# Kernel tuning notes

Hardware: AMD Instinct MI355X
Metric: run time of the kernel (lower is better)

## Reference

```python
import jax, jax.numpy as jnp
import numpy as np

HEADS = 16
DIM_HEAD = 64
QUERY_DIM = 1024
INNER = HEADS * DIM_HEAD
SCALE = DIM_HEAD ** -0.5


def setup_inputs() -> dict:
    key = jax.random.key(0)
    ks = jax.random.split(key, 6)
    B, N, M = 2, 2048, 2048
    x = jax.random.normal(ks[0], (B, N, QUERY_DIM), dtype=jnp.float32)
    context = jax.random.normal(ks[1], (B, M, QUERY_DIM), dtype=jnp.float32)
    s = QUERY_DIM ** -0.5
    # weights stored [in, out] so y = x @ W matches torch Linear(x) with W = weight.T
    Wq = jax.random.normal(ks[2], (QUERY_DIM, INNER), dtype=jnp.float32) * s
    Wk = jax.random.normal(ks[3], (QUERY_DIM, INNER), dtype=jnp.float32) * s
    Wv = jax.random.normal(ks[4], (QUERY_DIM, INNER), dtype=jnp.float32) * s
    Wo = jax.random.normal(ks[5], (INNER, QUERY_DIM), dtype=jnp.float32) * (INNER ** -0.5)
    return {"x": x, "context": context, "Wq": Wq, "Wk": Wk, "Wv": Wv, "Wo": Wo}


def reference(x, context, Wq, Wk, Wv, Wo):
    B, N, _ = x.shape
    M = context.shape[1]
    # projections -> [b, n, h, d]
    q = (x @ Wq).reshape(B, N, HEADS, DIM_HEAD)
    k = (context @ Wk).reshape(B, M, HEADS, DIM_HEAD)
    v = (context @ Wv).reshape(B, M, HEADS, DIM_HEAD)
    sim = jnp.einsum('bihd,bjhd->bhij', q, k) * SCALE  # [b, h, n, m]
    attn = jax.nn.softmax(sim, axis=-1)
    out = jnp.einsum('bhij,bjhd->bihd', attn, v)  # [b, n, h, d]
    out = out.reshape(B, N, INNER)
    return out @ Wo
```

## Files before the change

kernel.cpp:

```cpp
#include <hip/hip_runtime.h>
#include <hip/hip_bf16.h>


typedef __attribute__((ext_vector_type(8))) __bf16    bf16x8;
typedef __attribute__((ext_vector_type(4))) __bf16    bf16x4;
typedef __attribute__((ext_vector_type(4))) float     f32x4;

#define B_    2
#define H_    16
#define N_    2048
#define M_    2048
#define D_    64
#define QD_   1024

#define QSCALE 0.18033688011112042f

__device__ __forceinline__ void gld16(const __bf16* g, __bf16* l) {
    __builtin_amdgcn_global_load_lds(
        (const __attribute__((address_space(1))) unsigned int*)(g),
        (__attribute__((address_space(3))) unsigned int*)(l), 16, 0, 0);
}

__global__ __launch_bounds__(256) void cvt2_f32_bf16(const float* __restrict__ x,
                                                     const float* __restrict__ ctx,
                                                     __bf16* __restrict__ xb,
                                                     __bf16* __restrict__ cb) {
    const float* src = blockIdx.y ? ctx : x;
    __bf16*      dst = blockIdx.y ? cb  : xb;
    int i = (blockIdx.x * 256 + threadIdx.x) * 4;
    float4 v = *reinterpret_cast<const float4*>(src + i);
    bf16x4 o;
    o.x = (__bf16)v.x; o.y = (__bf16)v.y; o.z = (__bf16)v.z; o.w = (__bf16)v.w;
    *reinterpret_cast<bf16x4*>(dst + i) = o;
}

__global__ __launch_bounds__(256) void transpose4_cvt(const float* __restrict__ w0,
                                                      const float* __restrict__ w1,
                                                      const float* __restrict__ w2,
                                                      const float* __restrict__ w3,
                                                      __bf16* __restrict__ t0,
                                                      __bf16* __restrict__ t1,
                                                      __bf16* __restrict__ t2,
                                                      __bf16* __restrict__ t3) {
    __shared__ float tile[64][65];
    const int z = blockIdx.z;
    const float* in = (z == 0) ? w0 : (z == 1) ? w1 : (z == 2) ? w2 : w3;
    __bf16*     out = (z == 0) ? t0 : (z == 1) ? t1 : (z == 2) ? t2 : t3;
    const int i0 = blockIdx.x * 64;
    const int o0 = blockIdx.y * 64;
    const int t  = threadIdx.x;
    const int r  = t >> 4;
    const int c4 = (t & 15) * 4;
#pragma unroll
    for (int p = 0; p < 4; ++p) {
        int row = p * 16 + r;
        float4 v = *reinterpret_cast<const float4*>(in + (size_t)(i0 + row) * QD_ + o0 + c4);
        tile[row][c4 + 0] = v.x; tile[row][c4 + 1] = v.y;
        tile[row][c4 + 2] = v.z; tile[row][c4 + 3] = v.w;
    }
    __syncthreads();
#pragma unroll
    for (int p = 0; p < 4; ++p) {
        int orow = p * 16 + r;
        bf16x4 o;
        o.x = (__bf16)tile[c4 + 0][orow];
        o.y = (__bf16)tile[c4 + 1][orow];
        o.z = (__bf16)tile[c4 + 2][orow];
        o.w = (__bf16)tile[c4 + 3][orow];
        *reinterpret_cast<bf16x4*>(out + (size_t)(o0 + orow) * QD_ + i0 + c4) = o;
    }
}

#define GEMM_BODY(A_, Bt_)                                                                     \
    __shared__ __align__(16) __bf16 Alds[2][128 * 32];                                         \
    __shared__ __align__(16) __bf16 Blds[2][128 * 32];                                         \
    const int tid  = threadIdx.x;                                                              \
    const int wid  = tid >> 6;                                                                 \
    const int lane = tid & 63;                                                                 \
    const int l15  = lane & 15;                                                                \
    const int lg   = lane >> 4;                                                                \
    const int wr   = wid >> 1;                                                                 \
    const int wc   = wid & 1;                                                                  \
    const int rowBase = blockIdx.x * 128;                                                      \
    const int colBase = blockIdx.y * 128;                                                      \
    const int srow = wid * 32 + (lane >> 2);                                                   \
    const int skc  = (lane & 3) * 8;                                                           \
    const __bf16* Ag  = A_  + (size_t)(rowBase + srow) * QD_ + skc;                            \
    const __bf16* Ag2 = Ag  + (size_t)16 * QD_;                                                \
    const __bf16* Bg  = Bt_ + (size_t)(colBase + srow) * QD_ + skc;                            \
    const __bf16* Bg2 = Bg  + (size_t)16 * QD_;                                                \
    const int sOff  = (wid * 32) * 32;                                                         \
    const int sOff2 = sOff + 16 * 32;                                                          \
    f32x4 acc[4][4] = {};                                                                      \
    gld16(Ag,  &Alds[0][sOff]);                                                                \
    gld16(Ag2, &Alds[0][sOff2]);                                                               \
    gld16(Bg,  &Blds[0][sOff]);                                                                \
    gld16(Bg2, &Blds[0][sOff2]);                                                               \
    __syncthreads();                                                                           \
    for (int t = 0; t < 32; t += 2) {                                                          \
        if (t + 1 < 32) {                                                                      \
            int kn = (t + 1) * 32;                                                             \
            gld16(Ag + kn,  &Alds[1][sOff]);                                                   \
            gld16(Ag2 + kn, &Alds[1][sOff2]);                                                  \
            gld16(Bg + kn,  &Blds[1][sOff]);                                                   \
            gld16(Bg2 + kn, &Blds[1][sOff2]);                                                  \
        }                                                                                      \
        GCOMPUTE(0)                                                                            \
        __syncthreads();                                                                       \
        if (t + 2 < 32) {                                                                      \
            int kn = (t + 2) * 32;                                                             \
            gld16(Ag + kn,  &Alds[0][sOff]);                                                   \
            gld16(Ag2 + kn, &Alds[0][sOff2]);                                                  \
            gld16(Bg + kn,  &Blds[0][sOff]);                                                   \
            gld16(Bg2 + kn, &Blds[0][sOff2]);                                                  \
        }                                                                                      \
        GCOMPUTE(1)                                                                            \
        __syncthreads();                                                                      \
    }

#define GCOMPUTE(BUF)                                                                          \
    {                                                                                          \
        bf16x8 a[4], b[4];                                                                     \
        _Pragma("unroll")                                                                      \
        for (int m = 0; m < 4; ++m)                                                            \
            a[m] = *reinterpret_cast<const bf16x8*>(&Alds[BUF][(wr * 64 + m * 16 + l15) * 32 + lg * 8]); \
        _Pragma("unroll")                                                                      \
        for (int n = 0; n < 4; ++n)                                                            \
            b[n] = *reinterpret_cast<const bf16x8*>(&Blds[BUF][(wc * 64 + n * 16 + l15) * 32 + lg * 8]); \
        _Pragma("unroll")                                                                      \
        for (int m = 0; m < 4; ++m)                                                            \
            _Pragma("unroll")                                                                  \
            for (int n = 0; n < 4; ++n)                                                        \
                acc[m][n] = __builtin_amdgcn_mfma_f32_16x16x32_bf16(a[m], b[n], acc[m][n], 0, 0, 0); \
    }

__global__ __launch_bounds__(256) void gemm_qkv(const __bf16* __restrict__ xb,
                                                const __bf16* __restrict__ cb,
                                                const __bf16* __restrict__ Wtq,
                                                const __bf16* __restrict__ Wtk,
                                                const __bf16* __restrict__ Wtv,
                                                __bf16* __restrict__ Qb,
                                                __bf16* __restrict__ Kb,
                                                __bf16* __restrict__ Vt) {
    const int z = blockIdx.z;
    const __bf16* Asel = (z == 0) ? xb : cb;
    const __bf16* Bsel = (z == 0) ? Wtq : (z == 1) ? Wtk : Wtv;
    GEMM_BODY(Asel, Bsel)
#pragma unroll
    for (int m = 0; m < 4; ++m)
#pragma unroll
        for (int n = 0; n < 4; ++n)
#pragma unroll
            for (int r = 0; r < 4; ++r) {
                int rr = rowBase + wr * 64 + m * 16 + lg * 4 + r;
                int cc = colBase + wc * 64 + n * 16 + l15;
                float v = acc[m][n][r];
                int b_ = rr >> 11, nn = rr & 2047, hh = cc >> 6, dd = cc & 63;
                if (z == 0) {
                    Qb[((size_t)(b_ * H_ + hh) * N_ + nn) * D_ + dd] = (__bf16)(v * QSCALE);
                } else if (z == 1) {
                    Kb[((size_t)(b_ * H_ + hh) * N_ + nn) * D_ + dd] = (__bf16)v;
                } else {
                    Vt[((size_t)(b_ * H_ + hh) * D_ + dd) * M_ + nn] = (__bf16)v;
                }
            }
}

__global__ __launch_bounds__(256) void gemm_out(const __bf16* __restrict__ AO,
                                                const __bf16* __restrict__ Wto,
                                                float* __restrict__ out) {
    GEMM_BODY(AO, Wto)
#pragma unroll
    for (int m = 0; m < 4; ++m)
#pragma unroll
        for (int n = 0; n < 4; ++n)
#pragma unroll
            for (int r = 0; r < 4; ++r) {
                int rr = rowBase + wr * 64 + m * 16 + lg * 4 + r;
                int cc = colBase + wc * 64 + n * 16 + l15;
                out[(size_t)rr * QD_ + cc] = acc[m][n][r];
            }
}

__global__ __launch_bounds__(512, 4) void attn_kernel(const __bf16* __restrict__ Q,
                                                      const __bf16* __restrict__ K,
                                                      const __bf16* __restrict__ Vt,
                                                      __bf16* __restrict__ AO) {
    __shared__ __align__(16) __bf16 Klds[2][4096];
    __shared__ __align__(16) __bf16 Vlds[2][4096];

    const int logical = (blockIdx.x & 7) * 64 + (blockIdx.x >> 3);
    const int qt   = logical & 15;
    const int bh   = logical >> 4;
    const int b    = bh >> 4;
    const int h    = bh & 15;
    const int wid  = threadIdx.x >> 6;
    const int lane = threadIdx.x & 63;
    const int l15  = lane & 15;
    const int lg   = lane >> 4;
    const int qbase = qt * 128 + wid * 16;

    const __bf16* Qp = Q  + ((size_t)bh * N_ + qbase) * D_;
    const __bf16* Kp = K  + (size_t)bh * M_ * D_;
    const __bf16* Vp = Vt + (size_t)bh * D_ * M_;

    const int rg   = lane >> 3;
    const int ch   = lane & 7;
    const int skw  = (rg & 3) | ((wid & 1) << 2);
    const int kc   = (ch ^ skw) << 3;
    const int vc   = (ch ^ rg) << 3;
    const int srow = wid * 8 + rg;
    const int ldst = wid * 512;

#define STAGE(BUF, KV0)                                                        \
    gld16(Kp + (size_t)((KV0) + srow) * D_ + kc, &Klds[BUF][ldst]);            \
    gld16(Vp + (size_t)srow * M_ + (KV0) + vc,  &Vlds[BUF][ldst]);

    const int rm0 = ((l15 >> 2) * 8) + (l15 & 3);
    const int sq  = (l15 & 7) << 3;
    const int ak00 = rm0 * 64 + (( 0 + lg * 8) ^ sq);
    const int ak01 = rm0 * 64 + ((32 + lg * 8) ^ sq);
    const int ak10 = ak00 + 256;
    const int ak11 = ak01 + 256;
    const int av0 = l15 * 64 + (( 0 + lg * 8) ^ sq);
    const int av1 = l15 * 64 + ((32 + lg * 8) ^ sq);

    bf16x8 qf0 = *reinterpret_cast<const bf16x8*>(Qp + (size_t)l15 * D_ +      lg * 8);
    bf16x8 qf1 = *reinterpret_cast<const bf16x8*>(Qp + (size_t)l15 * D_ + 32 + lg * 8);

    bf16x8 onesf;
#pragma unroll
    for (int j = 0; j < 8; ++j) onesf[j] = (__bf16)1.0f;

    f32x4 o0 = {}, o1 = {}, o2 = {}, o3 = {}, ors = {};

#define COMPUTE(KB, VB, KOFF, AV)                                                               \
    {                                                                                           \
        bf16x8 k00 = *reinterpret_cast<const bf16x8*>((KB) + ak00 + (KOFF));                    \
        bf16x8 k01 = *reinterpret_cast<const bf16x8*>((KB) + ak01 + (KOFF));                    \
        bf16x8 k10 = *reinterpret_cast<const bf16x8*>((KB) + ak10 + (KOFF));                    \
        bf16x8 k11 = *reinterpret_cast<const bf16x8*>((KB) + ak11 + (KOFF));                    \
        bf16x8 v0  = *reinterpret_cast<const bf16x8*>((VB) + (AV));                             \
        bf16x8 v1  = *reinterpret_cast<const bf16x8*>((VB) + (AV) + 1024);                      \
        bf16x8 v2  = *reinterpret_cast<const bf16x8*>((VB) + (AV) + 2048);                      \
        bf16x8 v3  = *reinterpret_cast<const bf16x8*>((VB) + (AV) + 3072);                      \
        f32x4 s0 = {}, s1 = {};                                                                 \
        s0 = __builtin_amdgcn_mfma_f32_16x16x32_bf16(k00, qf0, s0, 0, 0, 0);                    \
        s0 = __builtin_amdgcn_mfma_f32_16x16x32_bf16(k01, qf1, s0, 0, 0, 0);                    \
        s1 = __builtin_amdgcn_mfma_f32_16x16x32_bf16(k10, qf0, s1, 0, 0, 0);                    \
        s1 = __builtin_amdgcn_mfma_f32_16x16x32_bf16(k11, qf1, s1, 0, 0, 0);                    \
        bf16x8 pf;                                                                              \
        pf[0] = (__bf16)__builtin_amdgcn_exp2f(s0[0]);                                          \
        pf[1] = (__bf16)__builtin_amdgcn_exp2f(s0[1]);                                          \
        pf[2] = (__bf16)__builtin_amdgcn_exp2f(s0[2]);                                          \
        pf[3] = (__bf16)__builtin_amdgcn_exp2f(s0[3]);                                          \
        pf[4] = (__bf16)__builtin_amdgcn_exp2f(s1[0]);                                          \
        pf[5] = (__bf16)__builtin_amdgcn_exp2f(s1[1]);                                          \
        pf[6] = (__bf16)__builtin_amdgcn_exp2f(s1[2]);                                          \
        pf[7] = (__bf16)__builtin_amdgcn_exp2f(s1[3]);                                          \
        ors = __builtin_amdgcn_mfma_f32_16x16x32_bf16(pf, onesf, ors, 0, 0, 0);                 \
        o0 = __builtin_amdgcn_mfma_f32_16x16x32_bf16(pf, v0, o0, 0, 0, 0);                      \
        o1 = __builtin_amdgcn_mfma_f32_16x16x32_bf16(pf, v1, o1, 0, 0, 0);                      \
        o2 = __builtin_amdgcn_mfma_f32_16x16x32_bf16(pf, v2, o2, 0, 0, 0);                      \
        o3 = __builtin_amdgcn_mfma_f32_16x16x32_bf16(pf, v3, o3, 0, 0, 0);                      \
    }

    STAGE(0, 0)
    __syncthreads();

    for (int t = 0; t < 32; t += 2) {
        if (t + 1 < 32) { STAGE(1, (t + 1) * 64) }
        COMPUTE(Klds[0], Vlds[0], 0,    av0)
        COMPUTE(Klds[0], Vlds[0], 2048, av1)
        __syncthreads();
        if (t + 2 < 32) { STAGE(0, (t + 2) * 64) }
        COMPUTE(Klds[1], Vlds[1], 0,    av0)
        COMPUTE(Klds[1], Vlds[1], 2048, av1)
        __syncthreads();
    }
#undef STAGE
#undef COMPUTE

#pragma unroll
    for (int r = 0; r < 4; ++r) {
        float inv = 1.0f / ors[r];
        size_t row = ((size_t)b * N_ + qbase + lg * 4 + r) * QD_ + h * D_ + l15;
        AO[row +  0] = (__bf16)(o0[r] * inv);
        AO[row + 16] = (__bf16)(o1[r] * inv);
        AO[row + 32] = (__bf16)(o2[r] * inv);
        AO[row + 48] = (__bf16)(o3[r] * inv);
    }
}

extern "C" void kernel_launch(void* const* d_in, const int* in_sizes, int n_in,
                              void* d_out, int out_size, void* d_ws, size_t ws_size,
                              hipStream_t stream) {
    const float* x   = (const float*)d_in[0];
    const float* ctx = (const float*)d_in[1];
    const float* Wq  = (const float*)d_in[2];
    const float* Wk  = (const float*)d_in[3];
    const float* Wv  = (const float*)d_in[4];
    const float* Wo  = (const float*)d_in[5];

    char* ws = (char*)d_ws;
    __bf16* xb  = (__bf16*)(ws);
    __bf16* cb  = (__bf16*)(ws + (8u  << 20));
    __bf16* Wtq = (__bf16*)(ws + (16u << 20));
    __bf16* Wtk = (__bf16*)(ws + (18u << 20));
    __bf16* Wtv = (__bf16*)(ws + (20u << 20));
    __bf16* Wto = (__bf16*)(ws + (22u << 20));
    __bf16* Qb  = (__bf16*)(ws + (24u << 20));
    __bf16* Kb  = (__bf16*)(ws + (32u << 20));
    __bf16* Vt  = (__bf16*)(ws + (40u << 20));
    __bf16* AO  = (__bf16*)(ws + (48u << 20));

    cvt2_f32_bf16<<<dim3(4096, 2), 256, 0, stream>>>(x, ctx, xb, cb);
    transpose4_cvt<<<dim3(16, 16, 4), 256, 0, stream>>>(Wq, Wk, Wv, Wo, Wtq, Wtk, Wtv, Wto);
    gemm_qkv<<<dim3(32, 8, 3), 256, 0, stream>>>(xb, cb, Wtq, Wtk, Wtv, Qb, Kb, Vt);
    attn_kernel<<<512, 512, 0, stream>>>(Qb, Kb, Vt, AO);
    gemm_out<<<dim3(32, 8), 256, 0, stream>>>(AO, Wto, (float*)d_out);
}
```

Before: 123.1 us.

## Load GEMM B fragments directly from global into registers and swizzle A LDS

The GEMM no longer stages the B (weight) tile through LDS. Each wave loads its B MFMA fragments straight from global memory into registers, double-buffered across k-steps. The A tile's LDS layout gains an XOR swizzle on the 16-byte column chunk to reduce bank conflicts on fragment reads. This halves LDS traffic and footprint, at the cost of redundant global B loads across the two row-waves and extra VGPR pressure.

After: 161.1 us. 1.31x slower.

```diff
diff --git a/kernel.cpp b/kernel.cpp
--- a/kernel.cpp
+++ b/kernel.cpp
@@ -73,7 +73,6 @@
 
 #define GEMM_BODY(A_, Bt_)                                                                     \
     __shared__ __align__(16) __bf16 Alds[2][128 * 32];                                         \
-    __shared__ __align__(16) __bf16 Blds[2][128 * 32];                                         \
     const int tid  = threadIdx.x;                                                              \
     const int wid  = tid >> 6;                                                                 \
     const int lane = tid & 63;                                                                 \
@@ -84,54 +83,65 @@
     const int rowBase = blockIdx.x * 128;                                                      \
     const int colBase = blockIdx.y * 128;                                                      \
     const int srow = wid * 32 + (lane >> 2);                                                   \
-    const int skc  = (lane & 3) * 8;                                                           \
-    const __bf16* Ag  = A_  + (size_t)(rowBase + srow) * QD_ + skc;                            \
-    const __bf16* Ag2 = Ag  + (size_t)16 * QD_;                                                \
-    const __bf16* Bg  = Bt_ + (size_t)(colBase + srow) * QD_ + skc;                            \
-    const __bf16* Bg2 = Bg  + (size_t)16 * QD_;                                                \
+    const int sg   = (((lane & 3) ^ ((srow >> 1) & 3))) * 8;     \
+    const __bf16* Ag  = A_  + (size_t)(rowBase + srow) * QD_ + sg;                             \
+    const __bf16* Ag2 = Ag  + (size_t)16 * QD_;           \
+    const __bf16* Bg  = Bt_ + (size_t)(colBase + wc * 64 + l15) * QD_ + lg * 8;                \
     const int sOff  = (wid * 32) * 32;                                                         \
     const int sOff2 = sOff + 16 * 32;                                                          \
+    int aoff[4];                                                                               \
+    _Pragma("unroll")                                                                          \
+    for (int m = 0; m < 4; ++m) {                                                              \
+        int row = wr * 64 + m * 16 + l15;                                                      \
+        aoff[m] = row * 32 + ((lg ^ ((row >> 1) & 3)) * 8);                                    \
+    }                                                                                          \
     f32x4 acc[4][4] = {};                                                                      \
+    bf16x8 bA0, bA1, bA2, bA3, bB0, bB1, bB2, bB3;                                             \
     gld16(Ag,  &Alds[0][sOff]);                                                                \
     gld16(Ag2, &Alds[0][sOff2]);                                                               \
-    gld16(Bg,  &Blds[0][sOff]);                                                                \
-    gld16(Bg2, &Blds[0][sOff2]);                                                               \
+    bA0 = *reinterpret_cast<const bf16x8*>(Bg);                                                \
+    bA1 = *reinterpret_cast<const bf16x8*>(Bg + (size_t)16 * QD_);                             \
+    bA2 = *reinterpret_cast<const bf16x8*>(Bg + (size_t)32 * QD_);                             \
+    bA3 = *reinterpret_cast<const bf16x8*>(Bg + (size_t)48 * QD_);                             \
     __syncthreads();                                                                           \
     for (int t = 0; t < 32; t += 2) {                                                          \
         if (t + 1 < 32) {                                                                      \
             int kn = (t + 1) * 32;                                                             \
             gld16(Ag + kn,  &Alds[1][sOff]);                                                   \
             gld16(Ag2 + kn, &Alds[1][sOff2]);                                                  \
-            gld16(Bg + kn,  &Blds[1][sOff]);                                                   \
-            gld16(Bg2 + kn, &Blds[1][sOff2]);                                                  \
+            bB0 = *reinterpret_cast<const bf16x8*>(Bg + kn);                                   \
+            bB1 = *reinterpret_cast<const bf16x8*>(Bg + (size_t)16 * QD_ + kn);                \
+            bB2 = *reinterpret_cast<const bf16x8*>(Bg + (size_t)32 * QD_ + kn);                \
+            bB3 = *reinterpret_cast<const bf16x8*>(Bg + (size_t)48 * QD_ + kn);                \
         }                                                                                      \
-        GCOMPUTE(0)                                                                            \
+        GCOMPUTE(0, bA0, bA1, bA2, bA3)                                                        \
         __syncthreads();                                                                       \
         if (t + 2 < 32) {                                                                      \
             int kn = (t + 2) * 32;                                                             \
             gld16(Ag + kn,  &Alds[0][sOff]);                                                   \
             gld16(Ag2 + kn, &Alds[0][sOff2]);                                                  \
-            gld16(Bg + kn,  &Blds[0][sOff]);                                                   \
-            gld16(Bg2 + kn, &Blds[0][sOff2]);                                                  \
+            bA0 = *reinterpret_cast<const bf16x8*>(Bg + kn);                                   \
+            bA1 = *reinterpret_cast<const bf16x8*>(Bg + (size_t)16 * QD_ + kn);                \
+            bA2 = *reinterpret_cast<const bf16x8*>(Bg + (size_t)32 * QD_ + kn);                \
+            bA3 = *reinterpret_cast<const bf16x8*>(Bg + (size_t)48 * QD_ + kn);                \
         }                                                                                      \
-        GCOMPUTE(1)                                                                            \
-        __syncthreads();                                                                      \
-    }
-
-#define GCOMPUTE(BUF)                                                                          \
+        GCOMPUTE(1, bB0, bB1, bB2, bB3)                                                        \
+        __syncthreads();                                                                       \
+    }
+
+#define GCOMPUTE(BUF, B0, B1, B2, B3)                                                          \
     {                                                                                          \
-        bf16x8 a[4], b[4];                                                                     \
+        bf16x8 a[4];                                                                           \
         _Pragma("unroll")                                                                      \
         for (int m = 0; m < 4; ++m)                                                            \
-            a[m] = *reinterpret_cast<const bf16x8*>(&Alds[BUF][(wr * 64 + m * 16 + l15) * 32 + lg * 8]); \
+            a[m] = *reinterpret_cast<const bf16x8*>(&Alds[BUF][aoff[m]]);                      \
         _Pragma("unroll")                                                                      \
-        for (int n = 0; n < 4; ++n)                                                            \
-            b[n] = *reinterpret_cast<const bf16x8*>(&Blds[BUF][(wc * 64 + n * 16 + l15) * 32 + lg * 8]); \
-        _Pragma("unroll")                                                                      \
-        for (int m = 0; m < 4; ++m)                                                            \
-            _Pragma("unroll")                                                                  \
-            for (int n = 0; n < 4; ++n)                                                        \
-                acc[m][n] = __builtin_amdgcn_mfma_f32_16x16x32_bf16(a[m], b[n], acc[m][n], 0, 0, 0); \
+        for (int m = 0; m < 4; ++m) {                                                          \
+            acc[m][0] = __builtin_amdgcn_mfma_f32_16x16x32_bf16(a[m], B0, acc[m][0], 0, 0, 0); \
+            acc[m][1] = __builtin_amdgcn_mfma_f32_16x16x32_bf16(a[m], B1, acc[m][1], 0, 0, 0); \
+            acc[m][2] = __builtin_amdgcn_mfma_f32_16x16x32_bf16(a[m], B2, acc[m][2], 0, 0, 0); \
+            acc[m][3] = __builtin_amdgcn_mfma_f32_16x16x32_bf16(a[m], B3, acc[m][3], 0, 0, 0); \
+        }                                                                                      \
     }
 
 __global__ __launch_bounds__(256) void gemm_qkv(const __bf16* __restrict__ xb,
```
